# Kernel tuning notes

Hardware: AMD Instinct MI355X
Metric: run time of the kernel (lower is better)

The kernel has to match this reference:

```python
import jax, jax.numpy as jnp
from jax import lax
import numpy as np


def setup_inputs() -> dict:
    key = jax.random.key(0)
    ks = jax.random.split(key, 10)
    B, C, T, H, W = 4, 128, 32, 24, 24
    M, k_t, k_s, mix_k = 3, 3, 3, 3
    s = 0.05
    q = jax.random.normal(ks[0], (B, C, T, H, W), jnp.float32)
    k = jax.random.normal(ks[1], (B, C, T, H, W), jnp.float32)
    v = jax.random.normal(ks[2], (B, C, T, H, W), jnp.float32)
    # depthwise 3D kernel banks: [M, C, 1, k_t, k_s, k_s] (OIDHW per branch, groups=C)
    Wk = jax.random.normal(ks[3], (M, C, 1, k_t, k_s, k_s), jnp.float32) * s
    Wv = jax.random.normal(ks[4], (M, C, 1, k_t, k_s, k_s), jnp.float32) * s
    # mix predictor: 1x1 conv1d (pointwise) + causal conv1d C->M
    pre_w = jax.random.normal(ks[5], (C, C), jnp.float32) * s
    pre_b = jax.random.normal(ks[6], (C,), jnp.float32) * s
    mix_w = jax.random.normal(ks[7], (M, C, mix_k), jnp.float32) * s
    mix_b = jax.random.normal(ks[8], (M,), jnp.float32) * s
    return {"q": q, "k": k, "v": v, "Wk": Wk, "Wv": Wv,
            "pre_w": pre_w, "pre_b": pre_b, "mix_w": mix_w, "mix_b": mix_b}


def _mix_alpha(q, pre_w, pre_b, mix_w, mix_b):
    # q: [B,C,T,H,W] -> global spatial pool -> [B,C,T]
    qg = q.mean(axis=(3, 4))
    h = jnp.einsum('oc,bct->bot', pre_w, qg) + pre_b[None, :, None]
    h = jax.nn.gelu(h, approximate=False)  # torch nn.GELU default = exact
    mix_k = mix_w.shape[-1]
    logits = lax.conv_general_dilated(
        h, mix_w, window_strides=(1,), padding=[(mix_k - 1, 0)],
        dimension_numbers=('NCH', 'OIH', 'NCH')) + mix_b[None, :, None]
    return jax.nn.softmax(logits, axis=1)  # [B,M,T]


def _dwconv3d_causal(x, w):
    # x: [B,C,T,H,W], w: [C,1,k_t,k_h,k_w] depthwise (groups=C)
    C = x.shape[1]
    k_t, k_h, k_w = w.shape[2], w.shape[3], w.shape[4]
    pad = [(k_t - 1, 0), (k_h // 2, k_h // 2), (k_w // 2, k_w // 2)]
    return lax.conv_general_dilated(
        x, w, window_strides=(1, 1, 1), padding=pad,
        dimension_numbers=('NCDHW', 'OIDHW', 'NCDHW'),
        feature_group_count=C)


def reference(q, k, v, Wk, Wv, pre_w, pre_b, mix_w, mix_b):
    alpha = _mix_alpha(q, pre_w, pre_b, mix_w, mix_b)  # [B,M,T]
    # all M depthwise branches at once: [M,B,C,T,H,W]
    km = jax.vmap(_dwconv3d_causal, in_axes=(None, 0))(k, Wk)
    vm = jax.vmap(_dwconv3d_causal, in_axes=(None, 0))(v, Wv)
    # per-time mixture-weighted sum over M
    k_out = jnp.einsum('mbcthw,bmt->bcthw', km, alpha)
    v_out = jnp.einsum('mbcthw,bmt->bcthw', vm, alpha)
    return (k_out, v_out)
```

## Files before the change

### kernel.cpp

```cpp
#include <hip/hip_runtime.h>
#include <math.h>

namespace {
constexpr int Bn = 4, Cn = 128, Tn = 32, Hn = 24, Wn = 24, Mn = 3;
constexpr int HWn = Hn * Wn;
constexpr int TTile = 8;
constexpr int PL = TTile + 2;
constexpr int RS = 28;
constexpr int PS = 26 * RS;
}

__global__ __launch_bounds__(256) void pool_kernel(const float* __restrict__ q,
                                                   float* __restrict__ qg) {
    int wave = threadIdx.x >> 6;
    int lane = threadIdx.x & 63;
    int plane = blockIdx.x * 4 + wave;
    const float4* p = (const float4*)(q + (size_t)plane * HWn);
    float4 a = p[lane];
    float4 b = p[lane + 64];
    float s = (a.x + a.y) + (a.z + a.w) + (b.x + b.y) + (b.z + b.w);
    if (lane < 16) {
        float4 c = p[128 + lane];
        s += (c.x + c.y) + (c.z + c.w);
    }
#pragma unroll
    for (int off = 32; off > 0; off >>= 1) s += __shfl_down(s, off);
    if (lane == 0) qg[plane] = s * (1.0f / 576.0f);
}

__global__ __launch_bounds__(512) void alpha_kernel(const float* __restrict__ qg,
                                                    const float* __restrict__ pre_w,
                                                    const float* __restrict__ pre_b,
                                                    const float* __restrict__ mix_w,
                                                    const float* __restrict__ mix_b,
                                                    float* __restrict__ alpha) {
    __shared__ float qg_s[Cn * Tn];
    __shared__ float h_s[Cn * (Tn + 2)];
    __shared__ float mw_s[Mn * Cn * 3];
    __shared__ float l_s[Mn * Tn];
    int b = blockIdx.x;
    int tid = threadIdx.x;
    for (int i = tid; i < Cn * Tn; i += 512) qg_s[i] = qg[b * Cn * Tn + i];
    for (int i = tid; i < Mn * Cn * 3; i += 512) mw_s[i] = mix_w[i];
    __syncthreads();
    {
        int o = tid >> 2;
        int t0 = (tid & 3) * 8;
        float bias = pre_b[o];
        float acc[8];
#pragma unroll
        for (int j = 0; j < 8; ++j) acc[j] = 0.f;
        const float* wrow = pre_w + o * Cn;
#pragma unroll 2
        for (int cb = 0; cb < Cn; cb += 8) {
            float wv[8];
#pragma unroll
            for (int j = 0; j < 8; ++j) wv[j] = wrow[cb + j];
#pragma unroll
            for (int j = 0; j < 8; ++j)
#pragma unroll
                for (int i = 0; i < 8; ++i)
                    acc[i] += wv[j] * qg_s[(cb + j) * Tn + t0 + i];
        }
        if ((tid & 3) == 0) { h_s[o * (Tn + 2) + 0] = 0.f; h_s[o * (Tn + 2) + 1] = 0.f; }
#pragma unroll
        for (int j = 0; j < 8; ++j) {
            float x = acc[j] + bias;
            h_s[o * (Tn + 2) + 2 + t0 + j] = 0.5f * x * (1.0f + erff(x * 0.70710678118654752f));
        }
    }
    __syncthreads();
    if (tid < Mn * Tn) {
        int m = tid / Tn, t = tid % Tn;
        float acc = mix_b[m];
#pragma unroll 8
        for (int c = 0; c < Cn; ++c) {
            const float* mw = mw_s + (m * Cn + c) * 3;
            const float* hp = h_s + c * (Tn + 2) + t;
            acc += mw[0] * hp[0] + mw[1] * hp[1] + mw[2] * hp[2];
        }
        l_s[m * Tn + t] = acc;
    }
    __syncthreads();
    if (tid < Tn) {
        int t = tid;
        float l0 = l_s[t], l1 = l_s[Tn + t], l2 = l_s[2 * Tn + t];
        float mx = fmaxf(l0, fmaxf(l1, l2));
        float e0 = expf(l0 - mx), e1 = expf(l1 - mx), e2 = expf(l2 - mx);
        float inv = 1.0f / (e0 + e1 + e2);
        alpha[(b * Mn + 0) * Tn + t] = e0 * inv;
        alpha[(b * Mn + 1) * Tn + t] = e1 * inv;
        alpha[(b * Mn + 2) * Tn + t] = e2 * inv;
    }
}

__global__ __launch_bounds__(384) void conv_kernel(const float* __restrict__ kin,
                                                   const float* __restrict__ vin,
                                                   const float* __restrict__ Wk,
                                                   const float* __restrict__ Wv,
                                                   const float* __restrict__ alpha,
                                                   float* __restrict__ out) {
    __shared__ float s[PL * PS];
    __shared__ float sw[TTile * 27];

    int bid = blockIdx.x;
    int tt = bid & 3;
    int c  = (bid >> 2) & 127;
    int b  = (bid >> 9) & 3;
    int br = bid >> 11;
    int t0 = tt * TTile;
    int tid = threadIdx.x;
    const size_t plane_base = (size_t)(b * Cn + c) * Tn;
    const float* __restrict__ src = br ? vin : kin;
    const float* __restrict__ Wb  = br ? Wv : Wk;

    float4 z4 = make_float4(0.f, 0.f, 0.f, 0.f);
    for (int i = tid; i < PL * PS / 4; i += 384) ((float4*)s)[i] = z4;
    __syncthreads();

    for (int idx = tid; idx < PL * 144; idx += 384) {
        int p = idx / 144;
        int cell = idx - p * 144;
        int r = cell / 6;
        int c4 = cell - r * 6;
        int tp = t0 - 2 + p;
        if (tp >= 0) {
            float4 val = *(const float4*)(src + (plane_base + tp) * HWn + r * 24 + c4 * 4);
            float* dst = s + p * PS + (r + 1) * RS + 1 + c4 * 4;
            dst[0] = val.x; dst[1] = val.y; dst[2] = val.z; dst[3] = val.w;
        }
    }
    if (tid < TTile * 27) {
        int tl = tid / 27;
        int widx = tid - tl * 27;
        float a0 = alpha[(b * Mn + 0) * Tn + t0 + tl];
        float a1 = alpha[(b * Mn + 1) * Tn + t0 + tl];
        float a2 = alpha[(b * Mn + 2) * Tn + t0 + tl];
        sw[tid] = a0 * Wb[(0 * Cn + c) * 27 + widx]
                + a1 * Wb[(1 * Cn + c) * 27 + widx]
                + a2 * Wb[(2 * Cn + c) * 27 + widx];
    }
    __syncthreads();

    int tl = tid / 48;
    int rem = tid - tl * 48;
    int h = rem >> 1;
    int w0 = (rem & 1) * 12;
    const float* wp = sw + tl * 27;
    float acc[12];
#pragma unroll
    for (int j = 0; j < 12; ++j) acc[j] = 0.f;
#pragma unroll
    for (int dt = 0; dt < 3; ++dt) {
#pragma unroll
        for (int dh = 0; dh < 3; ++dh) {
            const float* rp = s + (tl + dt) * PS + (h + dh) * RS + w0;
            float bf[14];
#pragma unroll
            for (int j = 0; j < 14; ++j) bf[j] = rp[j];
#pragma unroll
            for (int dw = 0; dw < 3; ++dw) {
                float wc = wp[dt * 9 + dh * 3 + dw];
#pragma unroll
                for (int j = 0; j < 12; ++j) acc[j] += bf[j + dw] * wc;
            }
        }
    }
    size_t obase = (plane_base + t0 + tl) * HWn + h * Wn + w0;
    float* op = out + (br ? (size_t)Bn * Cn * Tn * HWn : 0) + obase;
#pragma unroll
    for (int j = 0; j < 3; ++j)
        ((float4*)op)[j] = make_float4(acc[4*j], acc[4*j+1], acc[4*j+2], acc[4*j+3]);
}

extern "C" void kernel_launch(void* const* d_in, const int* in_sizes, int n_in,
                              void* d_out, int out_size, void* d_ws, size_t ws_size,
                              hipStream_t stream) {
    const float* q     = (const float*)d_in[0];
    const float* k     = (const float*)d_in[1];
    const float* v     = (const float*)d_in[2];
    const float* Wk    = (const float*)d_in[3];
    const float* Wv    = (const float*)d_in[4];
    const float* pre_w = (const float*)d_in[5];
    const float* pre_b = (const float*)d_in[6];
    const float* mix_w = (const float*)d_in[7];
    const float* mix_b = (const float*)d_in[8];
    float* out = (float*)d_out;

    float* qg    = (float*)d_ws;
    float* alpha = qg + Bn * Cn * Tn;

    hipLaunchKernelGGL(pool_kernel, dim3(Bn * Cn * Tn / 4), dim3(256), 0, stream, q, qg);
    hipLaunchKernelGGL(alpha_kernel, dim3(Bn), dim3(512), 0, stream,
                       qg, pre_w, pre_b, mix_w, mix_b, alpha);
    hipLaunchKernelGGL(conv_kernel, dim3(2 * Bn * Cn * (Tn / TTile)), dim3(384), 0, stream,
                       k, v, Wk, Wv, alpha, out);
}
```

Before: 216.4 us.

## Use XOR-swizzled float4 shared tile with fused zero-padding in depthwise conv

Changes the shared-memory halo tile to a 32-float row stride with XOR-swizzled float4 columns. Each thread now writes full float4s, including zeros for the padding, so the separate zero-fill pass and its barrier go away. The compute loop reads five swizzled float4s per row instead of fourteen scalar loads, cutting LDS instruction count and bank conflicts. Thread mapping changes so each wave half covers contiguous rows, and an occupancy hint of 6 is added to launch bounds, which may cap registers.

```diff
diff --git a/kernel.cpp b/kernel.cpp
--- a/kernel.cpp
+++ b/kernel.cpp
@@ -6,8 +6,9 @@
 constexpr int HWn = Hn * Wn;
 constexpr int TTile = 8;
 constexpr int PL = TTile + 2;
-constexpr int RS = 28;
-constexpr int PS = 26 * RS;
+constexpr int RSf = 32;
+constexpr int PRows = 26;
+constexpr int PSf = PRows * RSf;
 }
 
 __global__ __launch_bounds__(256) void pool_kernel(const float* __restrict__ q,
@@ -94,13 +95,13 @@
     }
 }
 
-__global__ __launch_bounds__(384) void conv_kernel(const float* __restrict__ kin,
-                                                   const float* __restrict__ vin,
-                                                   const float* __restrict__ Wk,
-                                                   const float* __restrict__ Wv,
-                                                   const float* __restrict__ alpha,
-                                                   float* __restrict__ out) {
-    __shared__ float s[PL * PS];
+__global__ __launch_bounds__(384, 6) void conv_kernel(const float* __restrict__ kin,
+                                                      const float* __restrict__ vin,
+                                                      const float* __restrict__ Wk,
+                                                      const float* __restrict__ Wv,
+                                                      const float* __restrict__ alpha,
+                                                      float* __restrict__ out) {
+    __shared__ float s[PL * PSf];
     __shared__ float sw[TTile * 27];
 
     int bid = blockIdx.x;
@@ -114,21 +115,17 @@
     const float* __restrict__ src = br ? vin : kin;
     const float* __restrict__ Wb  = br ? Wv : Wk;
 
-    float4 z4 = make_float4(0.f, 0.f, 0.f, 0.f);
-    for (int i = tid; i < PL * PS / 4; i += 384) ((float4*)s)[i] = z4;
-    __syncthreads();
-
-    for (int idx = tid; idx < PL * 144; idx += 384) {
-        int p = idx / 144;
-        int cell = idx - p * 144;
-        int r = cell / 6;
-        int c4 = cell - r * 6;
-        int tp = t0 - 2 + p;
-        if (tp >= 0) {
-            float4 val = *(const float4*)(src + (plane_base + tp) * HWn + r * 24 + c4 * 4);
-            float* dst = s + p * PS + (r + 1) * RS + 1 + c4 * 4;
-            dst[0] = val.x; dst[1] = val.y; dst[2] = val.z; dst[3] = val.w;
-        }
+    for (int idx = tid; idx < PL * PRows * 8; idx += 384) {
+        int p    = idx / (PRows * 8);
+        int rem2 = idx - p * (PRows * 8);
+        int rs   = rem2 >> 3;
+        int jp   = rem2 & 7;
+        int jl   = jp ^ (rs & 7);
+        int tp   = t0 - 2 + p;
+        float4 val = make_float4(0.f, 0.f, 0.f, 0.f);
+        if (tp >= 0 && (unsigned)(rs - 1) < 24u && (unsigned)(jl - 1) < 6u)
+            val = *(const float4*)(src + (plane_base + tp) * HWn + (rs - 1) * 24 + (jl - 1) * 4);
+        *(float4*)(s + p * PSf + rs * RSf + jp * 4) = val;
     }
     if (tid < TTile * 27) {
         int tl = tid / 27;
@@ -142,27 +139,40 @@
     }
     __syncthreads();
 
-    int tl = tid / 48;
+    int tl  = tid / 48;
     int rem = tid - tl * 48;
-    int h = rem >> 1;
-    int w0 = (rem & 1) * 12;
-    const float* wp = sw + tl * 27;
+    int sH  = rem / 24;
+    int h   = rem - sH * 24;
+    int w0  = sH * 12;
+    int cBase = 3 * sH;
+    const float* wrow = sw + tl * 27;
     float acc[12];
 #pragma unroll
     for (int j = 0; j < 12; ++j) acc[j] = 0.f;
 #pragma unroll
     for (int dt = 0; dt < 3; ++dt) {
+        const float* pp = s + (tl + dt) * PSf;
+        float wd[9];
+#pragma unroll
+        for (int j = 0; j < 9; ++j) wd[j] = wrow[dt * 9 + j];
 #pragma unroll
         for (int dh = 0; dh < 3; ++dh) {
-            const float* rp = s + (tl + dt) * PS + (h + dh) * RS + w0;
-            float bf[14];
-#pragma unroll
-            for (int j = 0; j < 14; ++j) bf[j] = rp[j];
+            int rs = h + dh;
+            const float* rp = pp + rs * RSf;
+            int key = rs & 7;
+            float bf[20];
+#pragma unroll
+            for (int cc = 0; cc < 5; ++cc) {
+                int jp = (cBase + cc) ^ key;
+                float4 t4 = *(const float4*)(rp + jp * 4);
+                bf[cc * 4 + 0] = t4.x; bf[cc * 4 + 1] = t4.y;
+                bf[cc * 4 + 2] = t4.z; bf[cc * 4 + 3] = t4.w;
+            }
 #pragma unroll
             for (int dw = 0; dw < 3; ++dw) {
-                float wc = wp[dt * 9 + dh * 3 + dw];
-#pragma unroll
-                for (int j = 0; j < 12; ++j) acc[j] += bf[j + dw] * wc;
+                float wc = wd[dh * 3 + dw];
+#pragma unroll
+                for (int j = 0; j < 12; ++j) acc[j] += bf[j + dw + 3] * wc;
             }
         }
     }
```

Result: slower. 273.0 us (+26.2%).
